# Kernel optimization log

Measured on AMD Instinct MI355X. Metric: run time of the kernel, lower is better.

Reference implementation:

```python
import jax, jax.numpy as jnp
import numpy as np

N = 50000      # nodes
E = 800000     # edges
F_IN = 5       # (E, X, Y, Z, T_rel)
D = 128        # hidden_dim
H = 4          # heads
C = D // H     # per-head channels = 32
L = 3          # num_gat_layers
NEG_SLOPE = 0.2


def setup_inputs() -> dict:
    key = jax.random.key(0)
    ks = jax.random.split(key, 20)
    s = 0.05
    inp = {
        "x": jax.random.normal(ks[0], (N, F_IN), dtype=jnp.float32),
        "edge_index": jax.random.randint(ks[1], (2, E), 0, N, dtype=jnp.int32),
        # node encoder
        "enc_W": jax.random.normal(ks[2], (F_IN, D), dtype=jnp.float32) * s,
        "enc_b": jnp.zeros((D,), jnp.float32),
        # stacked GATv2 params for L layers
        "Wl": jax.random.normal(ks[3], (L, D, D), dtype=jnp.float32) * s,
        "bl": jnp.zeros((L, D), jnp.float32),
        "Wr": jax.random.normal(ks[4], (L, D, D), dtype=jnp.float32) * s,
        "br": jnp.zeros((L, D), jnp.float32),
        "att": jax.random.normal(ks[5], (L, H, C), dtype=jnp.float32) * s,
        "gat_bias": jnp.zeros((L, D), jnp.float32),
        # edge classifier MLP (258 -> 128 -> 64 -> 1)
        "c1_W": jax.random.normal(ks[6], (2 * D + 2, D), dtype=jnp.float32) * s,
        "c1_b": jnp.zeros((D,), jnp.float32),
        "c2_W": jax.random.normal(ks[7], (D, 64), dtype=jnp.float32) * s,
        "c2_b": jnp.zeros((64,), jnp.float32),
        "c3_W": jax.random.normal(ks[8], (64, 1), dtype=jnp.float32) * s,
        "c3_b": jnp.zeros((1,), jnp.float32),
    }
    return inp


def _gatv2_layer(h, src, dst, Wl, bl, Wr, br, att, bias):
    # GATv2Conv (PyG semantics, share_weights=False, concat=True, self-loops added)
    xl = (h @ Wl + bl).reshape(N, H, C)   # source transform
    xr = (h @ Wr + br).reshape(N, H, C)   # target transform
    e = jax.nn.leaky_relu(xl[src] + xr[dst], NEG_SLOPE)      # [E', H, C]
    alpha = jnp.einsum("ehc,hc->eh", e, att)                 # [E', H]
    # scatter-softmax over incoming edges of each dst node (numerically stable)
    amax = jax.ops.segment_max(alpha, dst, num_segments=N)
    alpha = jnp.exp(alpha - amax[dst])
    denom = jax.ops.segment_sum(alpha, dst, num_segments=N)
    alpha = alpha / (denom[dst] + 1e-16)
    msg = xl[src] * alpha[:, :, None]                        # [E', H, C]
    out = jax.ops.segment_sum(msg, dst, num_segments=N)      # [N, H, C]
    return out.reshape(N, D) + bias


def reference(x, edge_index, enc_W, enc_b, Wl, bl, Wr, br, att, gat_bias,
              c1_W, c1_b, c2_W, c2_b, c3_W, c3_b):
    h = jax.nn.relu(x @ enc_W + enc_b)
    # add self-loops (PyG GATv2Conv default add_self_loops=True)
    loops = jnp.arange(N, dtype=edge_index.dtype)
    src = jnp.concatenate([edge_index[0], loops])
    dst = jnp.concatenate([edge_index[1], loops])
    for i in range(L):
        h = jax.nn.elu(_gatv2_layer(h, src, dst, Wl[i], bl[i], Wr[i], br[i], att[i], gat_bias[i]))
    # edge feature head on ORIGINAL edges
    row, col = edge_index[0], edge_index[1]
    ni = h[row]                                              # [E, D]
    nj = h[col]                                              # [E, D]
    delta_t = jnp.abs(x[row, 4] - x[col, 4])[:, None]        # [E, 1]
    dist = jnp.sqrt(jnp.sum((x[row, 1:4] - x[col, 1:4]) ** 2, axis=1))[:, None]
    ef = jnp.concatenate([ni, nj, delta_t, dist], axis=1)    # [E, 2D+2]
    o = jax.nn.relu(ef @ c1_W + c1_b)
    o = jax.nn.relu(o @ c2_W + c2_b)
    o = o @ c3_W + c3_b
    return o.reshape(-1)
```

## Files before the change

### kernel.cpp

```cpp
#include <hip/hip_runtime.h>
#include <hip/hip_bf16.h>

#define N_NODES 50000
#define N_EDGES 800000
#define DIM 128
#define NLAYER 3
#define NEG 0.2f

typedef __attribute__((ext_vector_type(8))) short short8;
typedef __attribute__((ext_vector_type(4))) float f32x4;

__global__ __launch_bounds__(256) void zero_kernel(int* p, int n) {
    int i = blockIdx.x * 256 + threadIdx.x;
    if (i < n) p[i] = 0;
}

__global__ __launch_bounds__(256) void hist_kernel(const int* __restrict__ dst, int* __restrict__ counts) {
    int e = blockIdx.x * 256 + threadIdx.x;
    if (e < N_EDGES) atomicAdd(&counts[dst[e]], 1);
}

__global__ __launch_bounds__(256) void scan1_kernel(const int* __restrict__ counts, int* __restrict__ indptr,
                                                    int* __restrict__ bsum, int n) {
    __shared__ int buf[256];
    int t = threadIdx.x;
    int i = blockIdx.x * 256 + t;
    int v = (i < n) ? counts[i] : 0;
    buf[t] = v;
    __syncthreads();
    for (int off = 1; off < 256; off <<= 1) {
        int add = (t >= off) ? buf[t - off] : 0;
        __syncthreads();
        buf[t] += add;
        __syncthreads();
    }
    if (i < n) indptr[i + 1] = buf[t];
    if (t == 255) bsum[blockIdx.x] = buf[255];
}

__global__ __launch_bounds__(256) void scan2_kernel(int* __restrict__ bsum, int* __restrict__ boff,
                                                    int* __restrict__ indptr, int nb) {
    __shared__ int buf[256];
    int t = threadIdx.x;
    int v = (t < nb) ? bsum[t] : 0;
    buf[t] = v;
    __syncthreads();
    for (int off = 1; off < 256; off <<= 1) {
        int add = (t >= off) ? buf[t - off] : 0;
        __syncthreads();
        buf[t] += add;
        __syncthreads();
    }
    if (t < nb) boff[t] = buf[t] - v;
    if (t == 0) indptr[0] = 0;
}

__global__ __launch_bounds__(256) void scan3_kernel(int* __restrict__ indptr, const int* __restrict__ boff, int n) {
    int i = blockIdx.x * 256 + threadIdx.x;
    if (i < n) indptr[i + 1] += boff[i >> 8];
}

__global__ __launch_bounds__(256) void place_kernel(const int* __restrict__ srcp, const int* __restrict__ dstp,
                                                    const int* __restrict__ indptr, int* __restrict__ cursor,
                                                    int* __restrict__ csr_src) {
    int e = blockIdx.x * 256 + threadIdx.x;
    if (e < N_EDGES) {
        int dn = dstp[e];
        int pos = indptr[dn] + atomicAdd(&cursor[dn], 1);
        csr_src[pos] = srcp[e];
    }
}

__global__ __launch_bounds__(256) void encoder_kernel(const float* __restrict__ x, const float* __restrict__ W,
                                                      const float* __restrict__ b, float* __restrict__ h) {
    int gid = blockIdx.x * 256 + threadIdx.x;
    int n = gid >> 7, d = gid & 127;
    if (n >= N_NODES) return;
    float acc = b[d];
#pragma unroll
    for (int f = 0; f < 5; f++) acc += x[n * 5 + f] * W[f * DIM + d];
    h[n * DIM + d] = fmaxf(acc, 0.f);
}

__global__ __launch_bounds__(256) void prep_weights_kernel(const float* __restrict__ Wl, const float* __restrict__ Wr,
                                                           const float* __restrict__ c1W,
                                                           unsigned short* __restrict__ wt) {
    int idx = blockIdx.x * 256 + threadIdx.x;
    int m = idx >> 14;
    int r = idx & 16383;
    int n = r >> 7, k = r & 127;
    int L = m >> 1, half = m & 1;
    const float* W;
    if (L < 3) W = (half ? Wr : Wl) + (size_t)L * 16384;
    else W = c1W + (size_t)half * 16384;
    float v = W[k * 128 + n];
    __hip_bfloat16 hb = __float2bfloat16(v);
    float rl = v - __bfloat162float(hb);
    __hip_bfloat16 lb = __float2bfloat16(rl);
    wt[(size_t)m * 32768 + n * 128 + k] = *reinterpret_cast<unsigned short*>(&hb);
    wt[(size_t)m * 32768 + 16384 + n * 128 + k] = *reinterpret_cast<unsigned short*>(&lb);
}

template <bool BF16OUT>
__global__ __launch_bounds__(256) void transform_mfma_kernel(const float* __restrict__ h,
                                                             const unsigned short* __restrict__ wtA,
                                                             const float* __restrict__ bA,
                                                             const unsigned short* __restrict__ wtB,
                                                             const float* __restrict__ bB,
                                                             void* __restrict__ outA_, void* __restrict__ outB_) {
    __shared__ __align__(16) char hhi[64 * 256];
    __shared__ __align__(16) char hlo[64 * 256];
    int t = threadIdx.x;
    int l = t & 63, w = t >> 6;
    int n0 = blockIdx.x * 64;
    for (int i = t; i < 64 * 32; i += 256) {
        int row = i >> 5, c4 = (i & 31) * 4;
        int n = n0 + row;
        float4 v = make_float4(0.f, 0.f, 0.f, 0.f);
        if (n < N_NODES) v = *(const float4*)&h[(size_t)n * DIM + c4];
        const float* pv = &v.x;
        unsigned short hi4[4], lo4[4];
#pragma unroll
        for (int q = 0; q < 4; q++) {
            __hip_bfloat16 hb = __float2bfloat16(pv[q]);
            float rl = pv[q] - __bfloat162float(hb);
            __hip_bfloat16 lb = __float2bfloat16(rl);
            hi4[q] = *reinterpret_cast<unsigned short*>(&hb);
            lo4[q] = *reinterpret_cast<unsigned short*>(&lb);
        }
        int addr = (row * 256 + c4 * 2) ^ ((row & 7) << 4);
        *(ushort4*)(hhi + addr) = make_ushort4(hi4[0], hi4[1], hi4[2], hi4[3]);
        *(ushort4*)(hlo + addr) = make_ushort4(lo4[0], lo4[1], lo4[2], lo4[3]);
    }
    __syncthreads();

    int lane_m = l & 15, lane_k8 = l >> 4;

#pragma unroll
    for (int mat = 0; mat < 2; mat++) {
        const short* wthi = (const short*)(mat ? wtB : wtA);
        const short* wtlo = wthi + 16384;
        const float* bias = mat ? bB : bA;
        short8 bh[2][4], bl_[2][4];
#pragma unroll
        for (int j = 0; j < 2; j++) {
            int nrow = (w * 2 + j) * 16 + lane_m;
#pragma unroll
            for (int ks = 0; ks < 4; ks++) {
                int ke = ks * 32 + lane_k8 * 8;
                bh[j][ks] = *(const short8*)(wthi + nrow * 128 + ke);
                bl_[j][ks] = *(const short8*)(wtlo + nrow * 128 + ke);
            }
        }
        f32x4 acc[4][2];
#pragma unroll
        for (int mt = 0; mt < 4; mt++)
#pragma unroll
            for (int j = 0; j < 2; j++) acc[mt][j] = (f32x4){0.f, 0.f, 0.f, 0.f};
#pragma unroll
        for (int ks = 0; ks < 4; ks++) {
            int kb = ks * 64 + lane_k8 * 16;
#pragma unroll
            for (int mt = 0; mt < 4; mt++) {
                int arow = mt * 16 + lane_m;
                int aswz = (arow & 7) << 4;
                short8 ahi = *(const short8*)(hhi + ((arow * 256 + kb) ^ aswz));
                short8 alo = *(const short8*)(hlo + ((arow * 256 + kb) ^ aswz));
#pragma unroll
                for (int j = 0; j < 2; j++) {
                    acc[mt][j] = __builtin_amdgcn_mfma_f32_16x16x32_bf16(ahi, bh[j][ks], acc[mt][j], 0, 0, 0);
                    acc[mt][j] = __builtin_amdgcn_mfma_f32_16x16x32_bf16(ahi, bl_[j][ks], acc[mt][j], 0, 0, 0);
                    acc[mt][j] = __builtin_amdgcn_mfma_f32_16x16x32_bf16(alo, bh[j][ks], acc[mt][j], 0, 0, 0);
                }
            }
        }
        void* outp = mat ? outB_ : outA_;
#pragma unroll
        for (int j = 0; j < 2; j++) {
            int col = (w * 2 + j) * 16 + lane_m;
            float bv = bias ? bias[col] : 0.f;
#pragma unroll
            for (int mt = 0; mt < 4; mt++) {
#pragma unroll
                for (int r = 0; r < 4; r++) {
                    int node = n0 + mt * 16 + lane_k8 * 4 + r;
                    if (node < N_NODES) {
                        float v = acc[mt][j][r] + bv;
                        if constexpr (BF16OUT) {
                            ((__hip_bfloat16*)outp)[(size_t)node * DIM + col] = __float2bfloat16(v);
                        } else {
                            ((float*)outp)[(size_t)node * DIM + col] = v;
                        }
                    }
                }
            }
        }
    }
}

__device__ __forceinline__ float edge_score(float4 v, float4 xrv, float4 attv) {
    float z, a;
    z = v.x + xrv.x; z = fmaxf(z, NEG * z); a = z * attv.x;
    z = v.y + xrv.y; z = fmaxf(z, NEG * z); a += z * attv.y;
    z = v.z + xrv.z; z = fmaxf(z, NEG * z); a += z * attv.z;
    z = v.w + xrv.w; z = fmaxf(z, NEG * z); a += z * attv.w;
    a += __shfl_xor(a, 1);
    a += __shfl_xor(a, 2);
    a += __shfl_xor(a, 4);
    return a;
}

__global__ __launch_bounds__(256) void gat_edge_kernel(const float* __restrict__ xl, const float* __restrict__ xr,
                                                       const float* __restrict__ att, const float* __restrict__ gbias,
                                                       const int* __restrict__ indptr, const int* __restrict__ csr_src,
                                                       float* __restrict__ h_out) {
    int n = blockIdx.x * 4 + (threadIdx.x >> 6);
    int l = threadIdx.x & 63;
    int half = l >> 5;
    int c0 = (l & 31) * 4;
    float4 xrv = *(const float4*)&xr[(size_t)n * DIM + c0];
    float4 attv = *(const float4*)&att[c0];
    int beg = indptr[n], end = indptr[n + 1];

    float m[2], den[2];
    float4 acc[2];
    {
        float4 v = *(const float4*)&xl[(size_t)n * DIM + c0];
        float a = edge_score(v, xrv, attv);
        if (half == 0) {
            m[0] = a; den[0] = 1.f; acc[0] = v;
        } else {
            m[0] = -3.4e38f; den[0] = 0.f; acc[0] = make_float4(0.f, 0.f, 0.f, 0.f);
        }
        m[1] = -3.4e38f; den[1] = 0.f; acc[1] = make_float4(0.f, 0.f, 0.f, 0.f);
    }

    for (int i = beg; i < end; i += 4) {
#pragma unroll
        for (int c = 0; c < 2; c++) {
            int idx = i + 2 * c + half;
            bool valid = idx < end;
            int s = valid ? csr_src[idx] : n;
            float4 v = *(const float4*)&xl[(size_t)s * DIM + c0];
            float a = edge_score(v, xrv, attv);
            if (!valid) a = -3.4e38f;
            float mn = fmaxf(m[c], a);
            float sc = __expf(m[c] - mn), p = __expf(a - mn);
            den[c] = den[c] * sc + p;
            acc[c].x = acc[c].x * sc + p * v.x;
            acc[c].y = acc[c].y * sc + p * v.y;
            acc[c].z = acc[c].z * sc + p * v.z;
            acc[c].w = acc[c].w * sc + p * v.w;
            m[c] = mn;
        }
    }
    {
        float mm = fmaxf(m[0], m[1]);
        float s0 = __expf(m[0] - mm), s1 = __expf(m[1] - mm);
        den[0] = den[0] * s0 + den[1] * s1;
        acc[0].x = acc[0].x * s0 + acc[1].x * s1;
        acc[0].y = acc[0].y * s0 + acc[1].y * s1;
        acc[0].z = acc[0].z * s0 + acc[1].z * s1;
        acc[0].w = acc[0].w * s0 + acc[1].w * s1;
        m[0] = mm;
    }
    {
        float mo = __shfl_xor(m[0], 32);
        float dno = __shfl_xor(den[0], 32);
        float4 ao;
        ao.x = __shfl_xor(acc[0].x, 32);
        ao.y = __shfl_xor(acc[0].y, 32);
        ao.z = __shfl_xor(acc[0].z, 32);
        ao.w = __shfl_xor(acc[0].w, 32);
        float mm = fmaxf(m[0], mo);
        float s0 = __expf(m[0] - mm), s1 = __expf(mo - mm);
        den[0] = den[0] * s0 + dno * s1;
        acc[0].x = acc[0].x * s0 + ao.x * s1;
        acc[0].y = acc[0].y * s0 + ao.y * s1;
        acc[0].z = acc[0].z * s0 + ao.z * s1;
        acc[0].w = acc[0].w * s0 + ao.w * s1;
    }
    if (half == 0) {
        float4 gb = *(const float4*)&gbias[c0];
        float inv = 1.f / (den[0] + 1e-16f);
        float4 o;
        o.x = acc[0].x * inv + gb.x;
        o.y = acc[0].y * inv + gb.y;
        o.z = acc[0].z * inv + gb.z;
        o.w = acc[0].w * inv + gb.w;
        o.x = (o.x > 0.f) ? o.x : __expf(o.x) - 1.f;
        o.y = (o.y > 0.f) ? o.y : __expf(o.y) - 1.f;
        o.z = (o.z > 0.f) ? o.z : __expf(o.z) - 1.f;
        o.w = (o.w > 0.f) ? o.w : __expf(o.w) - 1.f;
        *(float4*)&h_out[(size_t)n * DIM + c0] = o;
    }
}

__global__ __launch_bounds__(256) void edge_mlp_kernel(const unsigned* __restrict__ g1u, const unsigned* __restrict__ g2u,
                                                       const float* __restrict__ x, const int* __restrict__ ei,
                                                       const float* __restrict__ W1tail,
                                                       const float* __restrict__ W2, const float* __restrict__ b2,
                                                       const float* __restrict__ W3, const float* __restrict__ b3,
                                                       float* __restrict__ out, int ntiles) {
    __shared__ __align__(16) char smO1[64 * 256];
    __shared__ __align__(16) char smW2T[64 * 256];
    __shared__ float smCw[2][128];
    __shared__ float smPart[4][64];
    __shared__ int rowi[2][64], coli[2][64];
    __shared__ float sdt[2][64], sdi[2][64];
    int t = threadIdx.x;
    int l = t & 63, w = t >> 6;
    int s4 = t & 15;
    int ebase = t >> 4;

    for (int idx = t; idx < 128 * 64; idx += 256) {
        int k = idx >> 6, n = idx & 63;
        __hip_bfloat16 bv = __float2bfloat16(W2[idx]);
        unsigned short us = *reinterpret_cast<unsigned short*>(&bv);
        int addr = (n * 256 + k * 2) ^ ((n & 7) << 4);
        *(unsigned short*)(smW2T + addr) = us;
    }
    if (t < 128) {
        smCw[0][t] = W1tail[t];
        smCw[1][t] = W1tail[128 + t];
    }
    float b3v = b3[0];
    float b2v = b2[w * 16 + (l & 15)];
    float w3v = W3[w * 16 + (l & 15)];
    int koff = (l >> 4) * 16;

    const uint4* g1t = (const uint4*)g1u;
    const uint4* g2t = (const uint4*)g2u;

    uint4 u1[4], u2[4];
    int cur = 0;

    int tile0 = blockIdx.x;
    if (tile0 < ntiles) {
        if (t < 64) {
            int ge = tile0 * 64 + t;
            int r = ei[ge], c = ei[N_EDGES + ge];
            rowi[0][t] = r; coli[0][t] = c;
            sdt[0][t] = fabsf(x[r * 5 + 4] - x[c * 5 + 4]);
            float dx = x[r * 5 + 1] - x[c * 5 + 1];
            float dy = x[r * 5 + 2] - x[c * 5 + 2];
            float dz = x[r * 5 + 3] - x[c * 5 + 3];
            sdi[0][t] = sqrtf(dx * dx + dy * dy + dz * dz);
        }
        __syncthreads();
#pragma unroll
        for (int p = 0; p < 4; p++) {
            int e = ebase + p * 16;
            u1[p] = g1t[(size_t)rowi[0][e] * 16 + s4];
            u2[p] = g2t[(size_t)coli[0][e] * 16 + s4];
        }
    }

    for (int tile = blockIdx.x; tile < ntiles; tile += gridDim.x) {
        int nxt = tile + gridDim.x;
        __syncthreads();
#pragma unroll
        for (int p = 0; p < 4; p++) {
            int e = ebase + p * 16;
            float dtv = sdt[cur][e], div = sdi[cur][e];
            unsigned uo[4];
            const unsigned* a1 = &u1[p].x;
            const unsigned* a2 = &u2[p].x;
#pragma unroll
            for (int q = 0; q < 4; q++) {
                int d = s4 * 8 + q * 2;
                float lo = __uint_as_float(a1[q] << 16) + __uint_as_float(a2[q] << 16) + dtv * smCw[0][d] + div * smCw[1][d];
                float hi = __uint_as_float(a1[q] & 0xffff0000u) + __uint_as_float(a2[q] & 0xffff0000u) +
                           dtv * smCw[0][d + 1] + div * smCw[1][d + 1];
                lo = fmaxf(lo, 0.f); hi = fmaxf(hi, 0.f);
                __hip_bfloat16 blo = __float2bfloat16(lo), bhi = __float2bfloat16(hi);
                unsigned short ulo = *reinterpret_cast<unsigned short*>(&blo);
                unsigned short uhi = *reinterpret_cast<unsigned short*>(&bhi);
                uo[q] = (unsigned)ulo | ((unsigned)uhi << 16);
            }
            int addr = (e * 256 + s4 * 16) ^ ((e & 7) << 4);
            *(uint4*)(smO1 + addr) = *(uint4*)uo;
        }
        if (nxt < ntiles && t < 64) {
            int b = cur ^ 1;
            int ge = nxt * 64 + t;
            int r = ei[ge], c = ei[N_EDGES + ge];
            rowi[b][t] = r; coli[b][t] = c;
            sdt[b][t] = fabsf(x[r * 5 + 4] - x[c * 5 + 4]);
            float dx = x[r * 5 + 1] - x[c * 5 + 1];
            float dy = x[r * 5 + 2] - x[c * 5 + 2];
            float dz = x[r * 5 + 3] - x[c * 5 + 3];
            sdi[b][t] = sqrtf(dx * dx + dy * dy + dz * dz);
        }
        __syncthreads();
        if (nxt < ntiles) {
            int b = cur ^ 1;
#pragma unroll
            for (int p = 0; p < 4; p++) {
                int e = ebase + p * 16;
                u1[p] = g1t[(size_t)rowi[b][e] * 16 + s4];
                u2[p] = g2t[(size_t)coli[b][e] * 16 + s4];
            }
        }
        f32x4 acc[4];
#pragma unroll
        for (int mt = 0; mt < 4; mt++) acc[mt] = (f32x4){0.f, 0.f, 0.f, 0.f};
        int nrow = w * 16 + (l & 15);
#pragma unroll
        for (int ks = 0; ks < 4; ks++) {
            short8 bfrag = *(const short8*)(smW2T + ((nrow * 256 + koff + ks * 64) ^ ((nrow & 7) << 4)));
#pragma unroll
            for (int mt = 0; mt < 4; mt++) {
                int mrow = mt * 16 + (l & 15);
                short8 afrag = *(const short8*)(smO1 + ((mrow * 256 + koff + ks * 64) ^ ((mrow & 7) << 4)));
                acc[mt] = __builtin_amdgcn_mfma_f32_16x16x32_bf16(afrag, bfrag, acc[mt], 0, 0, 0);
            }
        }
        float p[4][4];
#pragma unroll
        for (int mt = 0; mt < 4; mt++)
#pragma unroll
            for (int r = 0; r < 4; r++) p[mt][r] = fmaxf(acc[mt][r] + b2v, 0.f) * w3v;
#pragma unroll
        for (int off = 8; off >= 1; off >>= 1)
#pragma unroll
            for (int mt = 0; mt < 4; mt++)
#pragma unroll
                for (int r = 0; r < 4; r++) p[mt][r] += __shfl_xor(p[mt][r], off);
        if ((l & 15) == 0) {
            int g = l >> 4;
#pragma unroll
            for (int mt = 0; mt < 4; mt++)
#pragma unroll
                for (int r = 0; r < 4; r++) smPart[w][mt * 16 + g * 4 + r] = p[mt][r];
        }
        __syncthreads();
        if (t < 64) out[tile * 64 + t] = smPart[0][t] + smPart[1][t] + smPart[2][t] + smPart[3][t] + b3v;
        cur ^= 1;
    }
}

extern "C" void kernel_launch(void* const* d_in, const int* in_sizes, int n_in,
                              void* d_out, int out_size, void* d_ws, size_t ws_size,
                              hipStream_t stream) {
    const float* x = (const float*)d_in[0];
    const int* ei = (const int*)d_in[1];
    const float* enc_W = (const float*)d_in[2];
    const float* enc_b = (const float*)d_in[3];
    const float* Wl = (const float*)d_in[4];
    const float* bl = (const float*)d_in[5];
    const float* Wr = (const float*)d_in[6];
    const float* br = (const float*)d_in[7];
    const float* att = (const float*)d_in[8];
    const float* gbias = (const float*)d_in[9];
    const float* c1_W = (const float*)d_in[10];
    const float* c1_b = (const float*)d_in[11];
    const float* c2_W = (const float*)d_in[12];
    const float* c2_b = (const float*)d_in[13];
    const float* c3_W = (const float*)d_in[14];
    const float* c3_b = (const float*)d_in[15];
    float* out = (float*)d_out;

    float* h = (float*)d_ws;
    float* xl = h + (size_t)N_NODES * DIM;
    float* xr = xl + (size_t)N_NODES * DIM;
    int* csr_src = (int*)(xr + (size_t)N_NODES * DIM);
    int* indptr = csr_src + N_EDGES;
    int* counts = indptr + (N_NODES + 1);
    int* bsum = counts + N_NODES;
    int* boff = bsum + 256;
    uintptr_t wp = (uintptr_t)(boff + 256);
    wp = (wp + 15) & ~(uintptr_t)15;
    unsigned short* wt = (unsigned short*)wp;

    const int* srcp = ei;
    const int* dstp = ei + N_EDGES;
    const int NB = (N_NODES + 255) / 256;
    const int TGRID = (N_NODES + 63) / 64;

    prep_weights_kernel<<<8 * 16384 / 256, 256, 0, stream>>>(Wl, Wr, c1_W, wt);

    zero_kernel<<<(N_NODES + 255) / 256, 256, 0, stream>>>(counts, N_NODES);
    hist_kernel<<<N_EDGES / 256, 256, 0, stream>>>(dstp, counts);
    scan1_kernel<<<NB, 256, 0, stream>>>(counts, indptr, bsum, N_NODES);
    scan2_kernel<<<1, 256, 0, stream>>>(bsum, boff, indptr, NB);
    scan3_kernel<<<NB, 256, 0, stream>>>(indptr, boff, N_NODES);
    zero_kernel<<<(N_NODES + 255) / 256, 256, 0, stream>>>(counts, N_NODES);
    place_kernel<<<N_EDGES / 256, 256, 0, stream>>>(srcp, dstp, indptr, counts, csr_src);

    encoder_kernel<<<(N_NODES * DIM) / 256, 256, 0, stream>>>(x, enc_W, enc_b, h);

    for (int i = 0; i < NLAYER; i++) {
        transform_mfma_kernel<false><<<TGRID, 256, 0, stream>>>(
            h, wt + (size_t)(i * 2) * 32768, bl + (size_t)i * DIM,
            wt + (size_t)(i * 2 + 1) * 32768, br + (size_t)i * DIM, xl, xr);
        gat_edge_kernel<<<N_NODES / 4, 256, 0, stream>>>(xl, xr, att + (size_t)i * DIM,
                                                         gbias + (size_t)i * DIM, indptr, csr_src, h);
    }

    transform_mfma_kernel<true><<<TGRID, 256, 0, stream>>>(
        h, wt + (size_t)6 * 32768, c1_b, wt + (size_t)7 * 32768, nullptr, xl, xr);

    edge_mlp_kernel<<<1024, 256, 0, stream>>>((const unsigned*)xl, (const unsigned*)xr, x, ei,
                                              c1_W + 256 * DIM, c2_W, c2_b, c3_W, c3_b, out, N_EDGES / 64);
}
```

Before: 596.3 us.

## Process edges in dst-sorted CSR order in MLP and widen GAT edge batching

```diff
diff --git a/kernel.cpp b/kernel.cpp
--- a/kernel.cpp
+++ b/kernel.cpp
@@ -62,12 +62,15 @@
 
 __global__ __launch_bounds__(256) void place_kernel(const int* __restrict__ srcp, const int* __restrict__ dstp,
                                                     const int* __restrict__ indptr, int* __restrict__ cursor,
-                                                    int* __restrict__ csr_src) {
+                                                    int* __restrict__ csr_src, int* __restrict__ csr_dst,
+                                                    int* __restrict__ csr_eid) {
     int e = blockIdx.x * 256 + threadIdx.x;
     if (e < N_EDGES) {
         int dn = dstp[e];
         int pos = indptr[dn] + atomicAdd(&cursor[dn], 1);
         csr_src[pos] = srcp[e];
+        csr_dst[pos] = dn;
+        csr_eid[pos] = e;
     }
 }
 
@@ -198,18 +201,6 @@
     }
 }
 
-__device__ __forceinline__ float edge_score(float4 v, float4 xrv, float4 attv) {
-    float z, a;
-    z = v.x + xrv.x; z = fmaxf(z, NEG * z); a = z * attv.x;
-    z = v.y + xrv.y; z = fmaxf(z, NEG * z); a += z * attv.y;
-    z = v.z + xrv.z; z = fmaxf(z, NEG * z); a += z * attv.z;
-    z = v.w + xrv.w; z = fmaxf(z, NEG * z); a += z * attv.w;
-    a += __shfl_xor(a, 1);
-    a += __shfl_xor(a, 2);
-    a += __shfl_xor(a, 4);
-    return a;
-}
-
 __global__ __launch_bounds__(256) void gat_edge_kernel(const float* __restrict__ xl, const float* __restrict__ xr,
                                                        const float* __restrict__ att, const float* __restrict__ gbias,
                                                        const int* __restrict__ indptr, const int* __restrict__ csr_src,
@@ -222,46 +213,75 @@
     float4 attv = *(const float4*)&att[c0];
     int beg = indptr[n], end = indptr[n + 1];
 
-    float m[2], den[2];
-    float4 acc[2];
+    float m[4], den[4];
+    float4 acc[4];
     {
         float4 v = *(const float4*)&xl[(size_t)n * DIM + c0];
-        float a = edge_score(v, xrv, attv);
+        float z, a;
+        z = v.x + xrv.x; z = fmaxf(z, NEG * z); a = z * attv.x;
+        z = v.y + xrv.y; z = fmaxf(z, NEG * z); a += z * attv.y;
+        z = v.z + xrv.z; z = fmaxf(z, NEG * z); a += z * attv.z;
+        z = v.w + xrv.w; z = fmaxf(z, NEG * z); a += z * attv.w;
+        a += __shfl_xor(a, 1);
+        a += __shfl_xor(a, 2);
+        a += __shfl_xor(a, 4);
         if (half == 0) {
             m[0] = a; den[0] = 1.f; acc[0] = v;
         } else {
             m[0] = -3.4e38f; den[0] = 0.f; acc[0] = make_float4(0.f, 0.f, 0.f, 0.f);
         }
-        m[1] = -3.4e38f; den[1] = 0.f; acc[1] = make_float4(0.f, 0.f, 0.f, 0.f);
-    }
-
-    for (int i = beg; i < end; i += 4) {
-#pragma unroll
-        for (int c = 0; c < 2; c++) {
+#pragma unroll
+        for (int c = 1; c < 4; c++) { m[c] = -3.4e38f; den[c] = 0.f; acc[c] = make_float4(0.f, 0.f, 0.f, 0.f); }
+    }
+
+    for (int i = beg; i < end; i += 8) {
+        int s[4];
+        bool val[4];
+        float4 v[4];
+        float a[4];
+#pragma unroll
+        for (int c = 0; c < 4; c++) {
             int idx = i + 2 * c + half;
-            bool valid = idx < end;
-            int s = valid ? csr_src[idx] : n;
-            float4 v = *(const float4*)&xl[(size_t)s * DIM + c0];
-            float a = edge_score(v, xrv, attv);
-            if (!valid) a = -3.4e38f;
-            float mn = fmaxf(m[c], a);
-            float sc = __expf(m[c] - mn), p = __expf(a - mn);
+            val[c] = idx < end;
+            s[c] = val[c] ? csr_src[idx] : n;
+        }
+#pragma unroll
+        for (int c = 0; c < 4; c++) v[c] = *(const float4*)&xl[(size_t)s[c] * DIM + c0];
+#pragma unroll
+        for (int c = 0; c < 4; c++) {
+            float z, aa;
+            z = v[c].x + xrv.x; z = fmaxf(z, NEG * z); aa = z * attv.x;
+            z = v[c].y + xrv.y; z = fmaxf(z, NEG * z); aa += z * attv.y;
+            z = v[c].z + xrv.z; z = fmaxf(z, NEG * z); aa += z * attv.z;
+            z = v[c].w + xrv.w; z = fmaxf(z, NEG * z); aa += z * attv.w;
+            a[c] = aa;
+        }
+#pragma unroll
+        for (int off = 1; off <= 4; off <<= 1)
+#pragma unroll
+            for (int c = 0; c < 4; c++) a[c] += __shfl_xor(a[c], off);
+#pragma unroll
+        for (int c = 0; c < 4; c++) {
+            if (!val[c]) a[c] = -3.4e38f;
+            float mn = fmaxf(m[c], a[c]);
+            float sc = __expf(m[c] - mn), p = __expf(a[c] - mn);
             den[c] = den[c] * sc + p;
-            acc[c].x = acc[c].x * sc + p * v.x;
-            acc[c].y = acc[c].y * sc + p * v.y;
-            acc[c].z = acc[c].z * sc + p * v.z;
-            acc[c].w = acc[c].w * sc + p * v.w;
+            acc[c].x = acc[c].x * sc + p * v[c].x;
+            acc[c].y = acc[c].y * sc + p * v[c].y;
+            acc[c].z = acc[c].z * sc + p * v[c].z;
+            acc[c].w = acc[c].w * sc + p * v[c].w;
             m[c] = mn;
         }
     }
-    {
-        float mm = fmaxf(m[0], m[1]);
-        float s0 = __expf(m[0] - mm), s1 = __expf(m[1] - mm);
-        den[0] = den[0] * s0 + den[1] * s1;
-        acc[0].x = acc[0].x * s0 + acc[1].x * s1;
-        acc[0].y = acc[0].y * s0 + acc[1].y * s1;
-        acc[0].z = acc[0].z * s0 + acc[1].z * s1;
-        acc[0].w = acc[0].w * s0 + acc[1].w * s1;
+#pragma unroll
+    for (int c = 1; c < 4; c++) {
+        float mm = fmaxf(m[0], m[c]);
+        float s0 = __expf(m[0] - mm), s1 = __expf(m[c] - mm);
+        den[0] = den[0] * s0 + den[c] * s1;
+        acc[0].x = acc[0].x * s0 + acc[c].x * s1;
+        acc[0].y = acc[0].y * s0 + acc[c].y * s1;
+        acc[0].z = acc[0].z * s0 + acc[c].z * s1;
+        acc[0].w = acc[0].w * s0 + acc[c].w * s1;
         m[0] = mm;
     }
     {
@@ -297,7 +317,9 @@
 }
 
 __global__ __launch_bounds__(256) void edge_mlp_kernel(const unsigned* __restrict__ g1u, const unsigned* __restrict__ g2u,
-                                                       const float* __restrict__ x, const int* __restrict__ ei,
+                                                       const float* __restrict__ x,
+                                                       const int* __restrict__ csr_src, const int* __restrict__ csr_dst,
+                                                       const int* __restrict__ csr_eid,
                                                        const float* __restrict__ W1tail,
                                                        const float* __restrict__ W2, const float* __restrict__ b2,
                                                        const float* __restrict__ W3, const float* __restrict__ b3,
@@ -306,12 +328,10 @@
     __shared__ __align__(16) char smW2T[64 * 256];
     __shared__ float smCw[2][128];
     __shared__ float smPart[4][64];
-    __shared__ int rowi[2][64], coli[2][64];
-    __shared__ float sdt[2][64], sdi[2][64];
+    __shared__ int rowi[64], coli[64], seid[64];
+    __shared__ float sdt[64], sdi[64];
     int t = threadIdx.x;
     int l = t & 63, w = t >> 6;
-    int s4 = t & 15;
-    int ebase = t >> 4;
 
     for (int idx = t; idx < 128 * 64; idx += 256) {
         int k = idx >> 6, n = idx & 63;
@@ -332,40 +352,28 @@
     const uint4* g1t = (const uint4*)g1u;
     const uint4* g2t = (const uint4*)g2u;
 
-    uint4 u1[4], u2[4];
-    int cur = 0;
-
-    int tile0 = blockIdx.x;
-    if (tile0 < ntiles) {
+    for (int tile = blockIdx.x; tile < ntiles; tile += gridDim.x) {
+        int p0 = tile * 64;
+        __syncthreads();
         if (t < 64) {
-            int ge = tile0 * 64 + t;
-            int r = ei[ge], c = ei[N_EDGES + ge];
-            rowi[0][t] = r; coli[0][t] = c;
-            sdt[0][t] = fabsf(x[r * 5 + 4] - x[c * 5 + 4]);
+            int p = p0 + t;
+            int r = csr_src[p], c = csr_dst[p];
+            rowi[t] = r; coli[t] = c; seid[t] = csr_eid[p];
+            sdt[t] = fabsf(x[r * 5 + 4] - x[c * 5 + 4]);
             float dx = x[r * 5 + 1] - x[c * 5 + 1];
             float dy = x[r * 5 + 2] - x[c * 5 + 2];
             float dz = x[r * 5 + 3] - x[c * 5 + 3];
-            sdi[0][t] = sqrtf(dx * dx + dy * dy + dz * dz);
-        }
-        __syncthreads();
-#pragma unroll
-        for (int p = 0; p < 4; p++) {
-            int e = ebase + p * 16;
-            u1[p] = g1t[(size_t)rowi[0][e] * 16 + s4];
-            u2[p] = g2t[(size_t)coli[0][e] * 16 + s4];
-        }
-    }
-
-    for (int tile = blockIdx.x; tile < ntiles; tile += gridDim.x) {
-        int nxt = tile + gridDim.x;
-        __syncthreads();
-#pragma unroll
-        for (int p = 0; p < 4; p++) {
-            int e = ebase + p * 16;
-            float dtv = sdt[cur][e], div = sdi[cur][e];
+            sdi[t] = sqrtf(dx * dx + dy * dy + dz * dz);
+        }
+        __syncthreads();
+        for (int idx = t; idx < 64 * 16; idx += 256) {
+            int e = idx >> 4, s4 = idx & 15;
+            uint4 u1 = g1t[(size_t)rowi[e] * 16 + s4];
+            uint4 u2 = g2t[(size_t)coli[e] * 16 + s4];
+            float dtv = sdt[e], div = sdi[e];
             unsigned uo[4];
-            const unsigned* a1 = &u1[p].x;
-            const unsigned* a2 = &u2[p].x;
+            const unsigned* a1 = &u1.x;
+            const unsigned* a2 = &u2.x;
 #pragma unroll
             for (int q = 0; q < 4; q++) {
                 int d = s4 * 8 + q * 2;
@@ -381,27 +389,7 @@
             int addr = (e * 256 + s4 * 16) ^ ((e & 7) << 4);
             *(uint4*)(smO1 + addr) = *(uint4*)uo;
         }
-        if (nxt < ntiles && t < 64) {
-            int b = cur ^ 1;
-            int ge = nxt * 64 + t;
-            int r = ei[ge], c = ei[N_EDGES + ge];
-            rowi[b][t] = r; coli[b][t] = c;
-            sdt[b][t] = fabsf(x[r * 5 + 4] - x[c * 5 + 4]);
-            float dx = x[r * 5 + 1] - x[c * 5 + 1];
-            float dy = x[r * 5 + 2] - x[c * 5 + 2];
-            float dz = x[r * 5 + 3] - x[c * 5 + 3];
-            sdi[b][t] = sqrtf(dx * dx + dy * dy + dz * dz);
-        }
-        __syncthreads();
-        if (nxt < ntiles) {
-            int b = cur ^ 1;
-#pragma unroll
-            for (int p = 0; p < 4; p++) {
-                int e = ebase + p * 16;
-                u1[p] = g1t[(size_t)rowi[b][e] * 16 + s4];
-                u2[p] = g2t[(size_t)coli[b][e] * 16 + s4];
-            }
-        }
+        __syncthreads();
         f32x4 acc[4];
 #pragma unroll
         for (int mt = 0; mt < 4; mt++) acc[mt] = (f32x4){0.f, 0.f, 0.f, 0.f};
@@ -435,8 +423,7 @@
                 for (int r = 0; r < 4; r++) smPart[w][mt * 16 + g * 4 + r] = p[mt][r];
         }
         __syncthreads();
-        if (t < 64) out[tile * 64 + t] = smPart[0][t] + smPart[1][t] + smPart[2][t] + smPart[3][t] + b3v;
-        cur ^= 1;
+        if (t < 64) out[seid[t]] = smPart[0][t] + smPart[1][t] + smPart[2][t] + smPart[3][t] + b3v;
     }
 }
 
@@ -465,7 +452,9 @@
     float* xl = h + (size_t)N_NODES * DIM;
     float* xr = xl + (size_t)N_NODES * DIM;
     int* csr_src = (int*)(xr + (size_t)N_NODES * DIM);
-    int* indptr = csr_src + N_EDGES;
+    int* csr_dst = csr_src + N_EDGES;
+    int* csr_eid = csr_dst + N_EDGES;
+    int* indptr = csr_eid + N_EDGES;
     int* counts = indptr + (N_NODES + 1);
     int* bsum = counts + N_NODES;
     int* boff = bsum + 256;
@@ -486,7 +475,7 @@
     scan2_kernel<<<1, 256, 0, stream>>>(bsum, boff, indptr, NB);
     scan3_kernel<<<NB, 256, 0, stream>>>(indptr, boff, N_NODES);
     zero_kernel<<<(N_NODES + 255) / 256, 256, 0, stream>>>(counts, N_NODES);
-    place_kernel<<<N_EDGES / 256, 256, 0, stream>>>(srcp, dstp, indptr, counts, csr_src);
+    place_kernel<<<N_EDGES / 256, 256, 0, stream>>>(srcp, dstp, indptr, counts, csr_src, csr_dst, csr_eid);
 
     encoder_kernel<<<(N_NODES * DIM) / 256, 256, 0, stream>>>(x, enc_W, enc_b, h);
 
@@ -501,6 +490,7 @@
     transform_mfma_kernel<true><<<TGRID, 256, 0, stream>>>(
         h, wt + (size_t)6 * 32768, c1_b, wt + (size_t)7 * 32768, nullptr, xl, xr);
 
-    edge_mlp_kernel<<<1024, 256, 0, stream>>>((const unsigned*)xl, (const unsigned*)xr, x, ei,
-                                              c1_W + 256 * DIM, c2_W, c2_b, c3_W, c3_b, out, N_EDGES / 64);
-}
+    edge_mlp_kernel<<<1024, 256, 0, stream>>>((const unsigned*)xl, (const unsigned*)xr, x,
+                                              csr_src, csr_dst, csr_eid, c1_W + 256 * DIM,
+                                              c2_W, c2_b, c3_W, c3_b, out, N_EDGES / 64);
+}
```

Measured after the change: 558.1 us. 6.4% less time.
